# Performance work log

Measured on AMD Instinct MI355X. Metric: run time of the kernel, lower is better.

The kernel has to match this reference:

```python
import jax, jax.numpy as jnp
import numpy as np

V, D, H, DK, DV = 60000, 300, 15, 20, 20
B, NH, NC, L = 128, 50, 5, 30
HD = H * DV  # 300, equals d_model
A = 200      # additive attention hidden dim


def _encode(x, Wq, Wk, Wv, Wp, bp, qv):
    # NRMS news/user encoder: MHSA over positions + additive attention pooling.
    # x: [B, L, D] -> [B, HD]
    b, l, _ = x.shape
    q = (x @ Wq).reshape(b, l, H, DK)
    k = (x @ Wk).reshape(b, l, H, DK)
    v = (x @ Wv).reshape(b, l, H, DV)
    scores = jnp.einsum('blhk,bmhk->bhlm', q, k) / jnp.sqrt(jnp.asarray(DK, x.dtype))
    attn = jax.nn.softmax(scores, axis=-1)
    ctx = jnp.einsum('bhlm,bmhv->blhv', attn, v).reshape(b, l, HD)
    a = jax.nn.softmax(jnp.tanh(ctx @ Wp + bp) @ qv, axis=-1)  # [b, l]
    return jnp.einsum('bl,blc->bc', a, ctx)

# vectorize over the per-position encoder axis (replaces the Python loop +
# incremental torch.cat): inputs [B, P, L, D], weights have leading dim P.
_encode_pos = jax.vmap(_encode, in_axes=(1, 0, 0, 0, 0, 0, 0), out_axes=1)


def setup_inputs() -> dict:
    key = jax.random.key(0)
    ks = jax.random.split(key, 24)

    def mk(k, shape, s=0.02):
        return s * jax.random.normal(k, shape, jnp.float32)

    inp = {
        'news_input': jax.random.randint(ks[0], (B, NH, L), 0, V),
        'candidates': jax.random.randint(ks[1], (B, NC, L), 0, V),
        'emb': mk(ks[2], (V, D), 0.1),
    }
    for name, n, base in [('his', NH, 3), ('cand', NC, 10), ('usr', 0, 17)]:
        sh = (n,) if n else ()
        kk = jax.random.split(ks[base], 6)
        inp[name + '_Wq'] = mk(kk[0], sh + (D, H * DK))
        inp[name + '_Wk'] = mk(kk[1], sh + (D, H * DK))
        inp[name + '_Wv'] = mk(kk[2], sh + (D, H * DV))
        inp[name + '_Wp'] = mk(kk[3], sh + (HD, A))
        inp[name + '_bp'] = mk(kk[4], sh + (A,))
        inp[name + '_qv'] = mk(kk[5], sh + (A,))
    return inp


def reference(news_input, candidates, emb,
              his_Wq, his_Wk, his_Wv, his_Wp, his_bp, his_qv,
              cand_Wq, cand_Wk, cand_Wv, cand_Wp, cand_bp, cand_qv,
              usr_Wq, usr_Wk, usr_Wv, usr_Wp, usr_bp, usr_qv):
    news_emb = emb[news_input]   # [B, 50, L, D]
    cand_emb = emb[candidates]   # [B, 5, L, D]
    news_enc = _encode_pos(news_emb, his_Wq, his_Wk, his_Wv, his_Wp, his_bp, his_qv)    # [B, 50, 300]
    cand_enc = _encode_pos(cand_emb, cand_Wq, cand_Wk, cand_Wv, cand_Wp, cand_bp, cand_qv)  # [B, 5, 300]
    user_rep = _encode(news_enc, usr_Wq, usr_Wk, usr_Wv, usr_Wp, usr_bp, usr_qv)        # [B, 300]
    scores = jnp.einsum('bd,bcd->bc', user_rep, cand_enc)  # bmm of [B,1,300] x [B,300,5]
    return jax.nn.softmax(scores, axis=-1)
```

## Files before the change

kernel.cpp:

```cpp
#include <hip/hip_runtime.h>
#include <math.h>

typedef __attribute__((ext_vector_type(8))) short short8;
typedef __attribute__((ext_vector_type(4))) short short4v;
typedef __attribute__((ext_vector_type(4))) float f32x4;

union U32S8 { unsigned u[4]; short8 s8; ushort e[8]; short4v h[2]; };

#define BATCH 128
#define NHIS  50
#define NCAND 5
#define KP    320
#define NQKV  1024
#define NWP   208
#define NQK   640
#define CTS   320
#define VOCAB 60000
#define SCALE 0.22360679774997896f

__device__ __forceinline__ ushort f2bf(float f) {
    union { float f; unsigned u; } v; v.f = f;
    return (ushort)((v.u + 0x7fffu + ((v.u >> 16) & 1u)) >> 16);
}
__device__ __forceinline__ unsigned pack2bf(float lo, float hi) {
    return (unsigned)f2bf(lo) | ((unsigned)f2bf(hi) << 16);
}
__device__ __forceinline__ float bf2f(ushort u) {
    union { float f; unsigned u; } v; v.u = ((unsigned)u) << 16;
    return v.f;
}

__device__ __forceinline__ void gl_lds16(const ushort* gsrc, ushort* ldst) {
    __builtin_amdgcn_global_load_lds(
        (const __attribute__((address_space(1))) unsigned int*)gsrc,
        (__attribute__((address_space(3))) unsigned int*)ldst,
        16, 0, 0);
}

__global__ void prep_emb(const float* __restrict__ emb, ushort* __restrict__ dst) {
    size_t gid = (size_t)blockIdx.x * 256 + threadIdx.x;
    size_t total8 = (size_t)VOCAB * (KP / 8);
    if (gid >= total8) return;
    size_t e0 = gid * 8;
    int row = (int)(e0 / KP);
    int c   = (int)(e0 - (size_t)row * KP);
    unsigned w[4] = {0, 0, 0, 0};
    if (c + 8 <= 300) {
        const float4* s = (const float4*)(emb + (size_t)row * 300 + c);
        float4 v0 = s[0], v1 = s[1];
        w[0] = pack2bf(v0.x, v0.y); w[1] = pack2bf(v0.z, v0.w);
        w[2] = pack2bf(v1.x, v1.y); w[3] = pack2bf(v1.z, v1.w);
    } else if (c < 300) {
        const float* s = emb + (size_t)row * 300;
        ushort tmp[8];
        #pragma unroll
        for (int i = 0; i < 8; ++i) tmp[i] = (c + i < 300) ? f2bf(s[c + i]) : (ushort)0;
        w[0] = tmp[0] | ((unsigned)tmp[1] << 16);
        w[1] = tmp[2] | ((unsigned)tmp[3] << 16);
        w[2] = tmp[4] | ((unsigned)tmp[5] << 16);
        w[3] = tmp[6] | ((unsigned)tmp[7] << 16);
    }
    *(unsigned*)(dst + e0)     = w[0];
    *(unsigned*)(dst + e0 + 2) = w[1];
    *(unsigned*)(dst + e0 + 4) = w[2];
    *(unsigned*)(dst + e0 + 6) = w[3];
}

__global__ void prep_qkv(const float* __restrict__ Wq, const float* __restrict__ Wk,
                         const float* __restrict__ Wv, ushort* __restrict__ dst, int P) {
    size_t i = (size_t)blockIdx.x * 256 + threadIdx.x;
    size_t total = (size_t)P * NQKV * KP;
    if (i >= total) return;
    int k = (int)(i % KP);
    int n = (int)((i / KP) % NQKV);
    int p = (int)(i / ((size_t)KP * NQKV));
    float v = 0.f;
    if (k < 300 && n < 900) {
        const float* W = (n < 300) ? Wq : (n < 600 ? Wk : Wv);
        int nn = n % 300;
        v = W[((size_t)p * 300 + k) * 300 + nn];
    }
    dst[i] = f2bf(v);
}

__global__ void prep_wp(const float* __restrict__ Wp, ushort* __restrict__ dst, int P) {
    size_t i = (size_t)blockIdx.x * 256 + threadIdx.x;
    size_t total = (size_t)P * NWP * KP;
    if (i >= total) return;
    int k = (int)(i % KP);
    int a = (int)((i / KP) % NWP);
    int p = (int)(i / ((size_t)KP * NWP));
    float v = 0.f;
    if (k < 300 && a < 200) v = Wp[((size_t)p * 300 + k) * 200 + a];
    dst[i] = f2bf(v);
}

template<int LQ, bool GATHER>
__global__ __launch_bounds__(256, 4)
void qkv_gemm(const ushort* __restrict__ src_bf,
              const int* __restrict__ tokens,
              const ushort* __restrict__ wt,
              ushort* __restrict__ qk, ushort* __restrict__ vt,
              int p0, int P_all, int NPMT)
{
    constexpr int MT = (LQ == 30) ? 30 : 50;
    constexpr int VS = (LQ == 30) ? 32 : 64;
    constexpr int TS = 136;

    __shared__ __align__(16) char SM[34816];
    __shared__ int TOK[128];

    const int group = blockIdx.x >> 6;
    const int w64   = blockIdx.x & 63;
    const int mt_g  = group * 8 + (w64 & 7);
    const int ntile = w64 >> 3;
    if (mt_g >= NPMT) return;
    const int mtile = mt_g % MT;
    const int p_l   = mt_g / MT;
    const int p_g   = p0 + p_l;
    const int t     = threadIdx.x;
    const int wave  = t >> 6, lane = t & 63;
    const int r = lane & 15, g = lane >> 4;
    const int qm = wave >> 1, qn = wave & 1;

    if (GATHER && t < 128) {
        int row = mtile * 128 + t;
        int b = row / LQ, l = row - b * LQ;
        TOK[t] = tokens[((size_t)b * P_all + p_g) * LQ + l];
    }
    __syncthreads();

    const int kcs   = (lane & 3) ^ ((lane >> 2) & 3);
    const int rowA0 = wave * 16 + (lane >> 2);
    const int rowA1 = 64 + rowA0;
    const ushort* wtp = wt + (size_t)p_g * NQKV * KP;

    const ushort *pA0, *pA1;
    if (GATHER) {
        pA0 = src_bf + (size_t)TOK[rowA0] * KP + kcs * 8;
        pA1 = src_bf + (size_t)TOK[rowA1] * KP + kcs * 8;
    } else {
        pA0 = src_bf + (size_t)(mtile * 128 + rowA0) * KP + kcs * 8;
        pA1 = src_bf + (size_t)(mtile * 128 + rowA1) * KP + kcs * 8;
    }
    const ushort* pB0 = wtp + (size_t)(ntile * 128 + rowA0) * KP + kcs * 8;
    const ushort* pB1 = wtp + (size_t)(ntile * 128 + rowA1) * KP + kcs * 8;

    auto stage = [&](int ks, int bufb) {
        int ko = ks * 32;
        char* base = SM + bufb * 8192;
        gl_lds16(pA0 + ko, (ushort*)(base + wave * 1024));
        gl_lds16(pA1 + ko, (ushort*)(base + 4096 + wave * 1024));
        char* baseB = SM + 16384 + bufb * 8192;
        gl_lds16(pB0 + ko, (ushort*)(baseB + wave * 1024));
        gl_lds16(pB1 + ko, (ushort*)(baseB + 4096 + wave * 1024));
    };

    f32x4 acc[4][4];
    #pragma unroll
    for (int i = 0; i < 4; ++i)
        #pragma unroll
        for (int j = 0; j < 4; ++j)
            acc[i][j] = (f32x4){0.f, 0.f, 0.f, 0.f};

    stage(0, 0);
    __syncthreads();
    int buf = 0;
    const int kx = g ^ (r & 3);
    for (int ks = 0; ks < 10; ++ks) {
        if (ks < 9) stage(ks + 1, buf ^ 1);
        const ushort* Ab = (const ushort*)(SM + buf * 8192);
        const ushort* Bb = (const ushort*)(SM + 16384 + buf * 8192);
        short8 af[4], bfr[4];
        #pragma unroll
        for (int fi = 0; fi < 4; ++fi)
            af[fi] = *(const short8*)&Ab[(qm * 64 + fi * 16 + r) * 32 + kx * 8];
        #pragma unroll
        for (int fj = 0; fj < 4; ++fj)
            bfr[fj] = *(const short8*)&Bb[(qn * 64 + fj * 16 + r) * 32 + kx * 8];
        #pragma unroll
        for (int fi = 0; fi < 4; ++fi)
            #pragma unroll
            for (int fj = 0; fj < 4; ++fj)
                acc[fi][fj] = __builtin_amdgcn_mfma_f32_16x16x32_bf16(af[fi], bfr[fj], acc[fi][fj], 0, 0, 0);
        __syncthreads();
        buf ^= 1;
    }

    ushort* T = (ushort*)SM;
    #pragma unroll
    for (int fi = 0; fi < 4; ++fi) {
        #pragma unroll
        for (int fj = 0; fj < 4; ++fj) {
            int col  = qn * 64 + fj * 16 + r;
            int rowb = qm * 64 + fi * 16 + 4 * g;
            #pragma unroll
            for (int j = 0; j < 4; ++j)
                T[(rowb + j) * TS + col] = f2bf(acc[fi][fj][j]);
        }
    }
    __syncthreads();

    const int R0 = mtile * 128;
    const int N0 = ntile * 128;
    ushort* qkp = qk + (size_t)p_l * (128 * MT) * NQK;
    ushort* vtp = vt + (size_t)p_l * BATCH * 15 * 20 * VS;

    {
        int nqk = 600 - N0;
        if (nqk > 128) nqk = 128;
        if (nqk > 0) {
            int nch = nqk >> 3;
            for (int t2 = t; t2 < 128 * nch; t2 += 256) {
                int row = t2 / nch, cc = t2 - row * nch;
                short8 v = *(const short8*)&T[row * TS + cc * 8];
                *(short8*)&qkp[(size_t)(R0 + row) * NQK + N0 + cc * 8] = v;
            }
        }
    }
    {
        int c0 = 600 - N0; if (c0 < 0) c0 = 0;
        int c1 = 900 - N0; if (c1 > 128) c1 = 128;
        if (c1 > c0) {
            int nvt = c1 - c0;
            int b0 = R0 / LQ, b1 = (R0 + 127) / LQ;
            int nb = b1 - b0 + 1;
            for (int t2 = t; t2 < nvt * nb; t2 += 256) {
                int ci = t2 % nvt, bi = t2 / nvt;
                int c = c0 + ci;
                int vj = N0 + c - 600;
                int h = vj / 20, jj = vj - h * 20;
                int b = b0 + bi;
                int gr0 = b * LQ;      if (gr0 < R0) gr0 = R0;
                int gr1 = b * LQ + LQ; if (gr1 > R0 + 128) gr1 = R0 + 128;
                if (gr1 <= gr0) continue;
                int l0 = gr0 - b * LQ, l1 = gr1 - b * LQ;
                ushort* dst = vtp + (((size_t)b * 15 + h) * 20 + jj) * VS;
                int l = l0;
                while (l < l1) {
                    if ((l & 7) == 0 && l + 8 <= l1) {
                        U32S8 v;
                        #pragma unroll
                        for (int i = 0; i < 8; ++i)
                            v.e[i] = T[(b * LQ + l + i - R0) * TS + c];
                        *(short8*)&dst[l] = v.s8;
                        l += 8;
                    } else if ((l & 1) == 0 && l + 2 <= l1) {
                        unsigned v = (unsigned)T[(b * LQ + l - R0) * TS + c] |
                                     ((unsigned)T[(b * LQ + l + 1 - R0) * TS + c] << 16);
                        *(unsigned*)&dst[l] = v;
                        l += 2;
                    } else {
                        dst[l] = T[(b * LQ + l - R0) * TS + c];
                        l += 1;
                    }
                }
            }
        }
    }
}

__device__ __forceinline__ short8 load_qk_frag(const ushort* rowptr, int colbase, int g, bool rowvalid) {
    U32S8 v;
    v.s8 = (short8){0,0,0,0,0,0,0,0};
    if (rowvalid && g < 3) {
        const ushort* src = rowptr + colbase;
        if (g < 2) {
            v.h[0] = *(const short4v*)src;
            v.h[1] = *(const short4v*)(src + 4);
        } else {
            v.h[0] = *(const short4v*)src;
        }
    }
    return v.s8;
}

template<bool BF16OUT>
__global__ __launch_bounds__(256, 4)
void attn_pool30(const ushort* __restrict__ qk,
                 const ushort* __restrict__ vt,
                 const ushort* __restrict__ wt_wp,
                 const float* __restrict__ bp, const float* __restrict__ qv,
                 float* __restrict__ outf, ushort* __restrict__ outbf,
                 int p0, int P_all)
{
    constexpr int CS = 328;
    __shared__ ushort C[32 * CS];
    __shared__ float  SL[32];
    __shared__ float  AW[32];

    const int tid  = threadIdx.x;
    const int wave = tid >> 6;
    const int lane = tid & 63;
    const int r = lane & 15, g = lane >> 4;
    const int p_l = blockIdx.x / BATCH;
    const int b   = blockIdx.x % BATCH;
    const int p_g = p0 + p_l;

    const ushort* qb  = qk + ((size_t)p_l * BATCH + b) * 30 * NQK;
    const ushort* vb  = vt + ((size_t)p_l * BATCH + b) * 15 * 640;
    const ushort* wpp = wt_wp + (size_t)p_g * NWP * KP;

    for (int i = tid; i < 32 * CS / 8; i += 256) {
        short8 z = (short8){0,0,0,0,0,0,0,0};
        *(short8*)&C[i * 8] = z;
    }
    if (tid < 32) SL[tid] = 0.f;
    __syncthreads();

    for (int hp = 0; hp < 4; ++hp) {
        int head = wave + 4 * hp;
        if (head < 15) {
            short8 q0 = load_qk_frag(qb + (size_t)(r) * NQK,      head * 20 + 8 * g, g, r < 30);
            short8 q1 = load_qk_frag(qb + (size_t)(16 + r) * NQK, head * 20 + 8 * g, g, 16 + r < 30);
            short8 k0 = load_qk_frag(qb + (size_t)(r) * NQK,      300 + head * 20 + 8 * g, g, r < 30);
            short8 k1 = load_qk_frag(qb + (size_t)(16 + r) * NQK, 300 + head * 20 + 8 * g, g, 16 + r < 30);
            short8 vf0 = *(const short8*)&vb[head * 640 + r * 32 + 8 * g];
            short8 vf1 = (16 + r < 20) ? *(const short8*)&vb[head * 640 + (16 + r) * 32 + 8 * g]
                                       : (short8){0,0,0,0,0,0,0,0};

            f32x4 s0m0 = {0,0,0,0}, s0m1 = {0,0,0,0}, s1m0 = {0,0,0,0}, s1m1 = {0,0,0,0};
            s0m0 = __builtin_amdgcn_mfma_f32_16x16x32_bf16(k0, q0, s0m0, 0, 0, 0);
            s0m1 = __builtin_amdgcn_mfma_f32_16x16x32_bf16(k1, q0, s0m1, 0, 0, 0);
            s1m0 = __builtin_amdgcn_mfma_f32_16x16x32_bf16(k0, q1, s1m0, 0, 0, 0);
            s1m1 = __builtin_amdgcn_mfma_f32_16x16x32_bf16(k1, q1, s1m1, 0, 0, 0);

            float mx0 = -1e30f, mx1 = -1e30f;
            #pragma unroll
            for (int j = 0; j < 4; ++j) {
                s0m0[j] *= SCALE; s1m0[j] *= SCALE;
                float v01 = (16 + 4 * g + j < 30) ? s0m1[j] * SCALE : -1e30f;
                float v11 = (16 + 4 * g + j < 30) ? s1m1[j] * SCALE : -1e30f;
                s0m1[j] = v01; s1m1[j] = v11;
                mx0 = fmaxf(mx0, fmaxf(s0m0[j], v01));
                mx1 = fmaxf(mx1, fmaxf(s1m0[j], v11));
            }
            mx0 = fmaxf(mx0, __shfl_xor(mx0, 16, 64));
            mx0 = fmaxf(mx0, __shfl_xor(mx0, 32, 64));
            mx1 = fmaxf(mx1, __shfl_xor(mx1, 16, 64));
            mx1 = fmaxf(mx1, __shfl_xor(mx1, 32, 64));
            float sm0 = 0.f, sm1 = 0.f;
            #pragma unroll
            for (int j = 0; j < 4; ++j) {
                s0m0[j] = __expf(s0m0[j] - mx0); s0m1[j] = __expf(s0m1[j] - mx0);
                s1m0[j] = __expf(s1m0[j] - mx1); s1m1[j] = __expf(s1m1[j] - mx1);
                sm0 += s0m0[j] + s0m1[j];
                sm1 += s1m0[j] + s1m1[j];
            }
            sm0 += __shfl_xor(sm0, 16, 64); sm0 += __shfl_xor(sm0, 32, 64);
            sm1 += __shfl_xor(sm1, 16, 64); sm1 += __shfl_xor(sm1, 32, 64);
            float inv0 = 1.0f / sm0, inv1 = 1.0f / sm1;

            unsigned pk000 = pack2bf(s0m0[0] * inv0, s0m0[1] * inv0);
            unsigned pk001 = pack2bf(s0m0[2] * inv0, s0m0[3] * inv0);
            unsigned pk010 = pack2bf(s0m1[0] * inv0, s0m1[1] * inv0);
            unsigned pk011 = pack2bf(s0m1[2] * inv0, s0m1[3] * inv0);
            unsigned pk100 = pack2bf(s1m0[0] * inv1, s1m0[1] * inv1);
            unsigned pk101 = pack2bf(s1m0[2] * inv1, s1m0[3] * inv1);
            unsigned pk110 = pack2bf(s1m1[0] * inv1, s1m1[1] * inv1);
            unsigned pk111 = pack2bf(s1m1[2] * inv1, s1m1[3] * inv1);

            const int sA = r + 16 * (2 * (g & 1));
            const int sB = sA + 16;
            const bool hi = (g >> 1) != 0;
            #pragma unroll
            for (int lt = 0; lt < 2; ++lt) {
                unsigned q00 = lt ? pk100 : pk000, q01 = lt ? pk101 : pk001;
                unsigned q10 = lt ? pk110 : pk010, q11 = lt ? pk111 : pk011;
                unsigned a0 = __shfl((int)q00, sA, 64), a1 = __shfl((int)q01, sA, 64);
                unsigned a2 = __shfl((int)q10, sA, 64), a3 = __shfl((int)q11, sA, 64);
                unsigned b0 = __shfl((int)q00, sB, 64), b1 = __shfl((int)q01, sB, 64);
                unsigned b2 = __shfl((int)q10, sB, 64), b3 = __shfl((int)q11, sB, 64);
                U32S8 pf;
                pf.u[0] = hi ? a2 : a0;
                pf.u[1] = hi ? a3 : a1;
                pf.u[2] = hi ? b2 : b0;
                pf.u[3] = hi ? b3 : b1;
                int lrow = lt * 16 + r;
                #pragma unroll
                for (int nt = 0; nt < 2; ++nt) {
                    short8 vf = nt ? vf1 : vf0;
                    f32x4 c = {0.f, 0.f, 0.f, 0.f};
                    c = __builtin_amdgcn_mfma_f32_16x16x32_bf16(vf, pf.s8, c, 0, 0, 0);
                    if (lrow < 30) {
                        #pragma unroll
                        for (int j = 0; j < 4; ++j) {
                            int vj = nt * 16 + 4 * g + j;
                            if (vj < 20)
                                C[lrow * CS + head * 20 + vj] = f2bf(c[j]);
                        }
                    }
                }
            }
        }
    }
    __syncthreads();

    for (int nt = wave; nt < 13; nt += 4) {
        int col = nt * 16 + r;
        const ushort* wrow = wpp + (size_t)col * KP + 8 * g;
        short8 breg[10];
        #pragma unroll
        for (int ks = 0; ks < 10; ++ks) breg[ks] = *(const short8*)(wrow + 32 * ks);
        float bpv = (col < 200) ? bp[p_g * 200 + col] : 0.f;
        float qvv = (col < 200) ? qv[p_g * 200 + col] : 0.f;

        f32x4 acc0 = {0.f, 0.f, 0.f, 0.f}, acc1 = {0.f, 0.f, 0.f, 0.f};
        #pragma unroll
        for (int ks = 0; ks < 10; ++ks) {
            short8 a0 = *(const short8*)&C[(r) * CS + ks * 32 + 8 * g];
            short8 a1 = *(const short8*)&C[(16 + r) * CS + ks * 32 + 8 * g];
            acc0 = __builtin_amdgcn_mfma_f32_16x16x32_bf16(a0, breg[ks], acc0, 0, 0, 0);
            acc1 = __builtin_amdgcn_mfma_f32_16x16x32_bf16(a1, breg[ks], acc1, 0, 0, 0);
        }
        #pragma unroll
        for (int j = 0; j < 4; ++j) {
            float s0 = tanhf(acc0[j] + bpv) * qvv;
            float s1 = tanhf(acc1[j] + bpv) * qvv;
            s0 += __shfl_xor(s0, 1, 64); s1 += __shfl_xor(s1, 1, 64);
            s0 += __shfl_xor(s0, 2, 64); s1 += __shfl_xor(s1, 2, 64);
            s0 += __shfl_xor(s0, 4, 64); s1 += __shfl_xor(s1, 4, 64);
            s0 += __shfl_xor(s0, 8, 64); s1 += __shfl_xor(s1, 8, 64);
            if (r == 0) {
                atomicAdd(&SL[4 * g + j], s0);
                atomicAdd(&SL[16 + 4 * g + j], s1);
            }
        }
    }
    __syncthreads();

    if (wave == 0) {
        float x = (lane < 30) ? SL[lane] : -1e30f;
        float mx = x;
        #pragma unroll
        for (int off = 1; off < 64; off <<= 1) mx = fmaxf(mx, __shfl_xor(mx, off, 64));
        float e = (lane < 30) ? __expf(x - mx) : 0.f;
        float sm = e;
        #pragma unroll
        for (int off = 1; off < 64; off <<= 1) sm += __shfl_xor(sm, off, 64);
        if (lane < 32) AW[lane] = e / sm;
    }
    __syncthreads();

    for (int c = tid; c < 300; c += 256) {
        float o = 0.f;
        #pragma unroll
        for (int l = 0; l < 30; ++l)
            o = fmaf(AW[l], bf2f(C[l * CS + c]), o);
        if (BF16OUT) outbf[((size_t)b * P_all + p_g) * KP + c] = f2bf(o);
        else         outf[((size_t)b * P_all + p_g) * 300 + c] = o;
    }
}

__global__ __launch_bounds__(512, 1)
void attn50(const ushort* __restrict__ qk,
            const ushort* __restrict__ vt,
            ushort* __restrict__ ctx)
{
    __shared__ ushort P_l[8][64 * 68];

    const int tid  = threadIdx.x;
    const int wave = tid >> 6;
    const int lane = tid & 63;
    const int r = lane & 15, g = lane >> 4;
    const int b = blockIdx.x;

    const ushort* qb = qk + (size_t)b * 50 * NQK;
    ushort* pw = &P_l[wave][0];

    for (int hh = wave; hh < 15; hh += 8) {
        short8 qf[4], kf[4];
        #pragma unroll
        for (int t4 = 0; t4 < 4; ++t4) {
            qf[t4] = load_qk_frag(qb + (size_t)(t4 * 16 + r) * NQK, hh * 20 + 8 * g, g, true);
            kf[t4] = load_qk_frag(qb + (size_t)(t4 * 16 + r) * NQK, 300 + hh * 20 + 8 * g, g, true);
        }
        short8 vf[2][2];
        #pragma unroll
        for (int nt = 0; nt < 2; ++nt) {
            int vj = nt * 16 + r;
            #pragma unroll
            for (int ks = 0; ks < 2; ++ks) {
                if (vj < 20)
                    vf[nt][ks] = *(const short8*)&vt[(((size_t)b * 15 + hh) * 20 + vj) * 64 + ks * 32 + 8 * g];
                else
                    vf[nt][ks] = (short8){0,0,0,0,0,0,0,0};
            }
        }

        f32x4 s[4][4];
        #pragma unroll
        for (int qt = 0; qt < 4; ++qt)
            #pragma unroll
            for (int kt = 0; kt < 4; ++kt) {
                f32x4 z = {0.f, 0.f, 0.f, 0.f};
                s[qt][kt] = __builtin_amdgcn_mfma_f32_16x16x32_bf16(kf[kt], qf[qt], z, 0, 0, 0);
            }

        float mx[4], sm[4];
        #pragma unroll
        for (int qt = 0; qt < 4; ++qt) {
            float m = -1e30f;
            #pragma unroll
            for (int kt = 0; kt < 4; ++kt)
                #pragma unroll
                for (int j = 0; j < 4; ++j) {
                    int col = kt * 16 + 4 * g + j;
                    float v = (col < 50) ? s[qt][kt][j] * SCALE : -1e30f;
                    s[qt][kt][j] = v;
                    m = fmaxf(m, v);
                }
            m = fmaxf(m, __shfl_xor(m, 16, 64));
            m = fmaxf(m, __shfl_xor(m, 32, 64));
            mx[qt] = m;
            float sum = 0.f;
            #pragma unroll
            for (int kt = 0; kt < 4; ++kt)
                #pragma unroll
                for (int j = 0; j < 4; ++j) {
                    float e = __expf(s[qt][kt][j] - m);
                    s[qt][kt][j] = e;
                    sum += e;
                }
            sum += __shfl_xor(sum, 16, 64);
            sum += __shfl_xor(sum, 32, 64);
            sm[qt] = 1.0f / sum;
        }

        #pragma unroll
        for (int qt = 0; qt < 4; ++qt) {
            float inv = sm[qt];
            #pragma unroll
            for (int kt = 0; kt < 4; ++kt) {
                unsigned w0 = pack2bf(s[qt][kt][0] * inv, s[qt][kt][1] * inv);
                unsigned w1 = pack2bf(s[qt][kt][2] * inv, s[qt][kt][3] * inv);
                ushort* dst = pw + (qt * 16 + r) * 68 + kt * 16 + 4 * g;
                *(unsigned*)dst = w0;
                *(unsigned*)(dst + 2) = w1;
            }
        }
        asm volatile("s_waitcnt lgkmcnt(0)");
        __builtin_amdgcn_sched_barrier(0);

        #pragma unroll
        for (int lt = 0; lt < 4; ++lt) {
            short8 pf0 = *(const short8*)(pw + (lt * 16 + r) * 68 + 8 * g);
            short8 pf1 = *(const short8*)(pw + (lt * 16 + r) * 68 + 32 + 8 * g);
            int l = lt * 16 + r;
            #pragma unroll
            for (int nt = 0; nt < 2; ++nt) {
                f32x4 c = {0.f, 0.f, 0.f, 0.f};
                c = __builtin_amdgcn_mfma_f32_16x16x32_bf16(vf[nt][0], pf0, c, 0, 0, 0);
                c = __builtin_amdgcn_mfma_f32_16x16x32_bf16(vf[nt][1], pf1, c, 0, 0, 0);
                int vjb = nt * 16 + 4 * g;
                if (l < 50 && vjb < 17) {
                    unsigned w0 = pack2bf(c[0], c[1]);
                    unsigned w1 = pack2bf(c[2], c[3]);
                    ushort* d = ctx + ((size_t)b * 64 + l) * CTS + hh * 20 + vjb;
                    *(unsigned*)d = w0;
                    *(unsigned*)(d + 2) = w1;
                }
            }
        }
    }
}

__global__ __launch_bounds__(256, 2)
void pool50(const ushort* __restrict__ ctx,
            const ushort* __restrict__ wt_wp,
            const float* __restrict__ bp, const float* __restrict__ qv,
            float* __restrict__ user_rep)
{
    __shared__ ushort Bt[2][208 * 40];
    __shared__ float  logit[128];
    __shared__ float  aw[128];

    const int tid  = threadIdx.x;
    const int wave = tid >> 6;
    const int lane = tid & 63;
    const int r = lane & 15, g = lane >> 4;

    const ushort* cbase = ctx + (size_t)blockIdx.x * 2 * 64 * CTS;

    auto stageB = [&](int ks, int buf) {
        for (int i = tid; i < 832; i += 256) {
            int n = i >> 2, kk = (i & 3) * 8;
            *(short8*)&Bt[buf][n * 40 + kk] = *(const short8*)&wt_wp[(size_t)n * KP + ks * 32 + kk];
        }
    };

    float bpr[13], qvr[13];
    #pragma unroll
    for (int nf = 0; nf < 13; ++nf) {
        int col = nf * 16 + r;
        bpr[nf] = (col < 200) ? bp[col] : 0.f;
        qvr[nf] = (col < 200) ? qv[col] : 0.f;
    }

    f32x4 acc[2][13];
    #pragma unroll
    for (int mf = 0; mf < 2; ++mf)
        #pragma unroll
        for (int nf = 0; nf < 13; ++nf)
            acc[mf][nf] = (f32x4){0.f, 0.f, 0.f, 0.f};

    stageB(0, 0);
    __syncthreads();
    int buf = 0;
    for (int ks = 0; ks < 10; ++ks) {
        if (ks < 9) stageB(ks + 1, buf ^ 1);
        short8 af[2];
        #pragma unroll
        for (int mf = 0; mf < 2; ++mf)
            af[mf] = *(const short8*)&cbase[(size_t)(wave * 32 + mf * 16 + r) * CTS + ks * 32 + 8 * g];
        #pragma unroll
        for (int mf = 0; mf < 2; ++mf)
            #pragma unroll
            for (int nf = 0; nf < 13; ++nf) {
                short8 bf = *(const short8*)&Bt[buf][(nf * 16 + r) * 40 + 8 * g];
                acc[mf][nf] = __builtin_amdgcn_mfma_f32_16x16x32_bf16(af[mf], bf, acc[mf][nf], 0, 0, 0);
            }
        __syncthreads();
        buf ^= 1;
    }

    #pragma unroll
    for (int mf = 0; mf < 2; ++mf) {
        #pragma unroll
        for (int j = 0; j < 4; ++j) {
            float s = 0.f;
            #pragma unroll
            for (int nf = 0; nf < 13; ++nf)
                s += tanhf(acc[mf][nf][j] + bpr[nf]) * qvr[nf];
            s += __shfl_xor(s, 1, 64);
            s += __shfl_xor(s, 2, 64);
            s += __shfl_xor(s, 4, 64);
            s += __shfl_xor(s, 8, 64);
            if (r == 0) logit[wave * 32 + mf * 16 + 4 * g + j] = s;
        }
    }
    __syncthreads();

    if (wave < 2) {
        float x = (lane < 50) ? logit[wave * 64 + lane] : -1e30f;
        float mx = x;
        #pragma unroll
        for (int off = 1; off < 64; off <<= 1) mx = fmaxf(mx, __shfl_xor(mx, off, 64));
        float e = (lane < 50) ? __expf(x - mx) : 0.f;
        float sm = e;
        #pragma unroll
        for (int off = 1; off < 64; off <<= 1) sm += __shfl_xor(sm, off, 64);
        aw[wave * 64 + lane] = e / sm;
    }
    __syncthreads();

    for (int idx = tid; idx < 2 * 300; idx += 256) {
        int inst = idx / 300, c = idx - inst * 300;
        const ushort* crow = cbase + (size_t)inst * 64 * CTS + c;
        float o = 0.f;
        #pragma unroll
        for (int l = 0; l < 50; ++l)
            o = fmaf(aw[inst * 64 + l], bf2f(crow[(size_t)l * CTS]), o);
        int b = blockIdx.x * 2 + inst;
        user_rep[(size_t)b * 300 + c] = o;
    }
}

__global__ __launch_bounds__(320)
void score_kernel(const float* __restrict__ user_rep, const float* __restrict__ cand_enc,
                  float* __restrict__ out)
{
    __shared__ float sc[NCAND];
    int b = blockIdx.x;
    int w = threadIdx.x >> 6;
    int lane = threadIdx.x & 63;
    float partial = 0.f;
    for (int d = lane; d < 300; d += 64)
        partial = fmaf(user_rep[b * 300 + d], cand_enc[((size_t)b * NCAND + w) * 300 + d], partial);
    for (int off = 32; off > 0; off >>= 1)
        partial += __shfl_down(partial, off, 64);
    if (lane == 0) sc[w] = partial;
    __syncthreads();
    if (threadIdx.x == 0) {
        float mx = -1e30f;
        for (int c = 0; c < NCAND; ++c) mx = fmaxf(mx, sc[c]);
        float s = 0.f; float e[NCAND];
        for (int c = 0; c < NCAND; ++c) { e[c] = __expf(sc[c] - mx); s += e[c]; }
        float inv = 1.0f / s;
        for (int c = 0; c < NCAND; ++c) out[b * NCAND + c] = e[c] * inv;
    }
}

extern "C" void kernel_launch(void* const* d_in, const int* in_sizes, int n_in,
                              void* d_out, int out_size, void* d_ws, size_t ws_size,
                              hipStream_t stream) {
    const int*   news_input = (const int*)d_in[0];
    const int*   candidates = (const int*)d_in[1];
    const float* emb        = (const float*)d_in[2];
    const float* his_Wq  = (const float*)d_in[3];
    const float* his_Wk  = (const float*)d_in[4];
    const float* his_Wv  = (const float*)d_in[5];
    const float* his_Wp  = (const float*)d_in[6];
    const float* his_bp  = (const float*)d_in[7];
    const float* his_qv  = (const float*)d_in[8];
    const float* cand_Wq = (const float*)d_in[9];
    const float* cand_Wk = (const float*)d_in[10];
    const float* cand_Wv = (const float*)d_in[11];
    const float* cand_Wp = (const float*)d_in[12];
    const float* cand_bp = (const float*)d_in[13];
    const float* cand_qv = (const float*)d_in[14];
    const float* usr_Wq  = (const float*)d_in[15];
    const float* usr_Wk  = (const float*)d_in[16];
    const float* usr_Wv  = (const float*)d_in[17];
    const float* usr_Wp  = (const float*)d_in[18];
    const float* usr_bp  = (const float*)d_in[19];
    const float* usr_qv  = (const float*)d_in[20];
    float* out = (float*)d_out;

    char* ws = (char*)d_ws;
    ushort* emb_bf      = (ushort*)ws;            ws += (size_t)VOCAB * KP * 2;
    ushort* news_enc_bf = (ushort*)ws;            ws += (size_t)BATCH * NHIS * KP * 2;
    float* cand_enc = (float*)ws;                 ws += (size_t)BATCH * NCAND * 300 * 4;
    float* user_rep = (float*)ws;                 ws += (size_t)BATCH * 300 * 4;
    ushort* his_qkvT  = (ushort*)ws;              ws += (size_t)NHIS * NQKV * KP * 2;
    ushort* his_wpT   = (ushort*)ws;              ws += (size_t)NHIS * NWP  * KP * 2;
    ushort* cand_qkvT = (ushort*)ws;              ws += (size_t)NCAND * NQKV * KP * 2;
    ushort* cand_wpT  = (ushort*)ws;              ws += (size_t)NCAND * NWP  * KP * 2;
    ushort* usr_qkvT  = (ushort*)ws;              ws += (size_t)NQKV * KP * 2;
    ushort* usr_wpT   = (ushort*)ws;              ws += (size_t)NWP  * KP * 2;

    size_t used = (size_t)(ws - (char*)d_ws);
    size_t avail = (ws_size > used) ? (ws_size - used) : 0;
    size_t qk_pp  = (size_t)3840 * NQK * 2;
    size_t vt_pp  = (size_t)BATCH * 15 * 640 * 2;
    size_t per_p  = qk_pp + vt_pp;
    int CP = (int)(avail / per_p);
    if (CP > 50) CP = 50;
    if (CP < 3) CP = 3;

    ushort* qk_ws  = (ushort*)ws;
    ushort* vt_ws  = qk_ws + (size_t)CP * 3840 * NQK;

    ushort* qk_u  = qk_ws;
    ushort* vt_u  = qk_u + (size_t)6400 * NQK;
    ushort* ctx_u = vt_u + (size_t)BATCH * 15 * 20 * 64;

    auto blocks = [](size_t total) { return (int)((total + 255) / 256); };
    auto qkv_grid = [](int npmt) { return ((npmt + 7) / 8) * 64; };

    hipMemsetAsync(news_enc_bf, 0, (size_t)BATCH * NHIS * KP * 2, stream);
    prep_emb<<<blocks((size_t)VOCAB * (KP / 8)), 256, 0, stream>>>(emb, emb_bf);
    prep_qkv<<<blocks((size_t)NHIS  * NQKV * KP), 256, 0, stream>>>(his_Wq,  his_Wk,  his_Wv,  his_qkvT,  NHIS);
    prep_qkv<<<blocks((size_t)NCAND * NQKV * KP), 256, 0, stream>>>(cand_Wq, cand_Wk, cand_Wv, cand_qkvT, NCAND);
    prep_qkv<<<blocks((size_t)1     * NQKV * KP), 256, 0, stream>>>(usr_Wq,  usr_Wk,  usr_Wv,  usr_qkvT,  1);
    prep_wp <<<blocks((size_t)NHIS  * NWP  * KP), 256, 0, stream>>>(his_Wp,  his_wpT,  NHIS);
    prep_wp <<<blocks((size_t)NCAND * NWP  * KP), 256, 0, stream>>>(cand_Wp, cand_wpT, NCAND);
    prep_wp <<<blocks((size_t)1     * NWP  * KP), 256, 0, stream>>>(usr_Wp,  usr_wpT,  1);

    for (int p0 = 0; p0 < NHIS; p0 += CP) {
        int cp = (NHIS - p0 < CP) ? (NHIS - p0) : CP;
        int npmt = cp * 30;
        qkv_gemm<30, true><<<qkv_grid(npmt), 256, 0, stream>>>(emb_bf, news_input, his_qkvT,
                                                               qk_ws, vt_ws, p0, NHIS, npmt);
        attn_pool30<true><<<cp * BATCH, 256, 0, stream>>>(qk_ws, vt_ws, his_wpT, his_bp, his_qv,
                                                          nullptr, news_enc_bf, p0, NHIS);
    }
    {
        int npmt = NCAND * 30;
        qkv_gemm<30, true><<<qkv_grid(npmt), 256, 0, stream>>>(emb_bf, candidates, cand_qkvT,
                                                               qk_ws, vt_ws, 0, NCAND, npmt);
        attn_pool30<false><<<NCAND * BATCH, 256, 0, stream>>>(qk_ws, vt_ws, cand_wpT, cand_bp, cand_qv,
                                                              cand_enc, nullptr, 0, NCAND);
    }

    hipMemsetAsync(vt_u, 0, (size_t)BATCH * 15 * 20 * 64 * 2, stream);
    qkv_gemm<50, false><<<qkv_grid(50), 256, 0, stream>>>(news_enc_bf, nullptr, usr_qkvT,
                                                          qk_u, vt_u, 0, 1, 50);
    attn50<<<BATCH, 512, 0, stream>>>(qk_u, vt_u, ctx_u);
    pool50<<<64, 256, 0, stream>>>(ctx_u, usr_wpT, usr_bp, usr_qv, user_rep);

    score_kernel<<<BATCH, 320, 0, stream>>>(user_rep, cand_enc, out);
}
```

Before: 804.8 us.

## Store Q and K in head-major contiguous layout for attention kernels

The QKV GEMM epilogue now writes Q and K into separate per-(batch, head) tiles of [L,20] bf16 instead of row-major [rows,640] with Q and K interleaved by column. The attention kernels (attn_pool30, attn50) read each head's Q/K fragments from contiguous 20-element rows, which should improve the locality of global loads. The intermediate footprint shrinks from 640 to 600 columns per row. In exchange, the epilogue scatter is more complex, with per-head vector-width branching and smaller stores.

```diff
diff --git a/kernel.cpp b/kernel.cpp
--- a/kernel.cpp
+++ b/kernel.cpp
@@ -13,7 +13,6 @@
 #define KP    320
 #define NQKV  1024
 #define NWP   208
-#define NQK   640
 #define CTS   320
 #define VOCAB 60000
 #define SCALE 0.22360679774997896f
@@ -35,6 +34,21 @@
         (const __attribute__((address_space(1))) unsigned int*)gsrc,
         (__attribute__((address_space(3))) unsigned int*)ldst,
         16, 0, 0);
+}
+
+__device__ __forceinline__ short8 load_h20(const ushort* tile20, int row, int g, bool rowvalid) {
+    U32S8 v;
+    v.s8 = (short8){0,0,0,0,0,0,0,0};
+    if (rowvalid && g < 3) {
+        const ushort* src = tile20 + row * 20 + 8 * g;
+        if (g < 2) {
+            v.h[0] = *(const short4v*)src;
+            v.h[1] = *(const short4v*)(src + 4);
+        } else {
+            v.h[0] = *(const short4v*)src;
+        }
+    }
+    return v.s8;
 }
 
 __global__ void prep_emb(const float* __restrict__ emb, ushort* __restrict__ dst) {
@@ -100,7 +114,7 @@
 void qkv_gemm(const ushort* __restrict__ src_bf,
               const int* __restrict__ tokens,
               const ushort* __restrict__ wt,
-              ushort* __restrict__ qk, ushort* __restrict__ vt,
+              ushort* __restrict__ qh, ushort* __restrict__ kh, ushort* __restrict__ vt,
               int p0, int P_all, int NPMT)
 {
     constexpr int MT = (LQ == 30) ? 30 : 50;
@@ -203,18 +217,52 @@
 
     const int R0 = mtile * 128;
     const int N0 = ntile * 128;
-    ushort* qkp = qk + (size_t)p_l * (128 * MT) * NQK;
+    ushort* qhp = qh + (size_t)p_l * BATCH * 15 * LQ * 20;
+    ushort* khp = kh + (size_t)p_l * BATCH * 15 * LQ * 20;
     ushort* vtp = vt + (size_t)p_l * BATCH * 15 * 20 * VS;
 
-    {
-        int nqk = 600 - N0;
-        if (nqk > 128) nqk = 128;
-        if (nqk > 0) {
-            int nch = nqk >> 3;
-            for (int t2 = t; t2 < 128 * nch; t2 += 256) {
-                int row = t2 / nch, cc = t2 - row * nch;
-                short8 v = *(const short8*)&T[row * TS + cc * 8];
-                *(short8*)&qkp[(size_t)(R0 + row) * NQK + N0 + cc * 8] = v;
+    #pragma unroll
+    for (int seg = 0; seg < 2; ++seg) {
+        int nlo = seg * 300;
+        int lo = (N0 > nlo) ? N0 : nlo;
+        int hi = ((N0 + 128) < (nlo + 300)) ? (N0 + 128) : (nlo + 300);
+        if (hi <= lo) continue;
+        int h0 = (lo - nlo) / 20;
+        int h1 = (hi - 1 - nlo) / 20;
+        int nh = h1 - h0 + 1;
+        ushort* dstb = seg ? khp : qhp;
+        for (int t2 = t; t2 < 128 * nh; t2 += 256) {
+            int hh = t2 % nh, row = t2 / nh;
+            int h = h0 + hh;
+            int nA = nlo + 20 * h;
+            int j0 = (lo > nA) ? (lo - nA) : 0;
+            int j1 = ((nA + 20) < hi ? (nA + 20) : hi) - nA;
+            int grow = R0 + row;
+            int b = grow / LQ, l = grow - b * LQ;
+            ushort* dst = dstb + (((size_t)b * 15 + h) * LQ + l) * 20;
+            const ushort* srcT = &T[row * TS + (nA + j0 - N0)];
+            int j = j0;
+            while (j < j1) {
+                if ((j & 7) == 0 && j + 8 <= j1) {
+                    U32S8 v;
+                    #pragma unroll
+                    for (int i = 0; i < 8; ++i) v.e[i] = srcT[j - j0 + i];
+                    *(short8*)&dst[j] = v.s8;
+                    j += 8;
+                } else if ((j & 3) == 0 && j + 4 <= j1) {
+                    U32S8 v;
+                    #pragma unroll
+                    for (int i = 0; i < 4; ++i) v.e[i] = srcT[j - j0 + i];
+                    *(short4v*)&dst[j] = v.h[0];
+                    j += 4;
+                } else if ((j & 1) == 0 && j + 2 <= j1) {
+                    unsigned v = (unsigned)srcT[j - j0] | ((unsigned)srcT[j - j0 + 1] << 16);
+                    *(unsigned*)&dst[j] = v;
+                    j += 2;
+                } else {
+                    dst[j] = srcT[j - j0];
+                    j += 1;
+                }
             }
         }
     }
@@ -260,24 +308,10 @@
     }
 }
 
-__device__ __forceinline__ short8 load_qk_frag(const ushort* rowptr, int colbase, int g, bool rowvalid) {
-    U32S8 v;
-    v.s8 = (short8){0,0,0,0,0,0,0,0};
-    if (rowvalid && g < 3) {
-        const ushort* src = rowptr + colbase;
-        if (g < 2) {
-            v.h[0] = *(const short4v*)src;
-            v.h[1] = *(const short4v*)(src + 4);
-        } else {
-            v.h[0] = *(const short4v*)src;
-        }
-    }
-    return v.s8;
-}
-
 template<bool BF16OUT>
 __global__ __launch_bounds__(256, 4)
-void attn_pool30(const ushort* __restrict__ qk,
+void attn_pool30(const ushort* __restrict__ qh,
+                 const ushort* __restrict__ kh,
                  const ushort* __restrict__ vt,
                  const ushort* __restrict__ wt_wp,
                  const float* __restrict__ bp, const float* __restrict__ qv,
@@ -297,7 +331,8 @@
     const int b   = blockIdx.x % BATCH;
     const int p_g = p0 + p_l;
 
-    const ushort* qb  = qk + ((size_t)p_l * BATCH + b) * 30 * NQK;
+    const ushort* qb  = qh + (((size_t)p_l * BATCH + b) * 15) * 600;
+    const ushort* kb  = kh + (((size_t)p_l * BATCH + b) * 15) * 600;
     const ushort* vb  = vt + ((size_t)p_l * BATCH + b) * 15 * 640;
     const ushort* wpp = wt_wp + (size_t)p_g * NWP * KP;
 
@@ -311,10 +346,12 @@
     for (int hp = 0; hp < 4; ++hp) {
         int head = wave + 4 * hp;
         if (head < 15) {
-            short8 q0 = load_qk_frag(qb + (size_t)(r) * NQK,      head * 20 + 8 * g, g, r < 30);
-            short8 q1 = load_qk_frag(qb + (size_t)(16 + r) * NQK, head * 20 + 8 * g, g, 16 + r < 30);
-            short8 k0 = load_qk_frag(qb + (size_t)(r) * NQK,      300 + head * 20 + 8 * g, g, r < 30);
-            short8 k1 = load_qk_frag(qb + (size_t)(16 + r) * NQK, 300 + head * 20 + 8 * g, g, 16 + r < 30);
+            const ushort* qt = qb + head * 600;
+            const ushort* kt = kb + head * 600;
+            short8 q0 = load_h20(qt, r, g, true);
+            short8 q1 = load_h20(qt, 16 + r, g, 16 + r < 30);
+            short8 k0 = load_h20(kt, r, g, true);
+            short8 k1 = load_h20(kt, 16 + r, g, 16 + r < 30);
             short8 vf0 = *(const short8*)&vb[head * 640 + r * 32 + 8 * g];
             short8 vf1 = (16 + r < 20) ? *(const short8*)&vb[head * 640 + (16 + r) * 32 + 8 * g]
                                        : (short8){0,0,0,0,0,0,0,0};
@@ -453,7 +490,8 @@
 }
 
 __global__ __launch_bounds__(512, 1)
-void attn50(const ushort* __restrict__ qk,
+void attn50(const ushort* __restrict__ qh,
+            const ushort* __restrict__ kh,
             const ushort* __restrict__ vt,
             ushort* __restrict__ ctx)
 {
@@ -465,15 +503,16 @@
     const int r = lane & 15, g = lane >> 4;
     const int b = blockIdx.x;
 
-    const ushort* qb = qk + (size_t)b * 50 * NQK;
     ushort* pw = &P_l[wave][0];
 
     for (int hh = wave; hh < 15; hh += 8) {
+        const ushort* qt = qh + (((size_t)b * 15 + hh) * 50) * 20;
+        const ushort* kt = kh + (((size_t)b * 15 + hh) * 50) * 20;
         short8 qf[4], kf[4];
         #pragma unroll
         for (int t4 = 0; t4 < 4; ++t4) {
-            qf[t4] = load_qk_frag(qb + (size_t)(t4 * 16 + r) * NQK, hh * 20 + 8 * g, g, true);
-            kf[t4] = load_qk_frag(qb + (size_t)(t4 * 16 + r) * NQK, 300 + hh * 20 + 8 * g, g, true);
+            qf[t4] = load_h20(qt, t4 * 16 + r, g, true);
+            kf[t4] = load_h20(kt, t4 * 16 + r, g, true);
         }
         short8 vf[2][2];
         #pragma unroll
@@ -490,51 +529,51 @@
 
         f32x4 s[4][4];
         #pragma unroll
-        for (int qt = 0; qt < 4; ++qt)
-            #pragma unroll
-            for (int kt = 0; kt < 4; ++kt) {
+        for (int qt2 = 0; qt2 < 4; ++qt2)
+            #pragma unroll
+            for (int kt2 = 0; kt2 < 4; ++kt2) {
                 f32x4 z = {0.f, 0.f, 0.f, 0.f};
-                s[qt][kt] = __builtin_amdgcn_mfma_f32_16x16x32_bf16(kf[kt], qf[qt], z, 0, 0, 0);
+                s[qt2][kt2] = __builtin_amdgcn_mfma_f32_16x16x32_bf16(kf[kt2], qf[qt2], z, 0, 0, 0);
             }
 
         float mx[4], sm[4];
         #pragma unroll
-        for (int qt = 0; qt < 4; ++qt) {
+        for (int qt2 = 0; qt2 < 4; ++qt2) {
             float m = -1e30f;
             #pragma unroll
-            for (int kt = 0; kt < 4; ++kt)
+            for (int kt2 = 0; kt2 < 4; ++kt2)
                 #pragma unroll
                 for (int j = 0; j < 4; ++j) {
-                    int col = kt * 16 + 4 * g + j;
-                    float v = (col < 50) ? s[qt][kt][j] * SCALE : -1e30f;
-                    s[qt][kt][j] = v;
+                    int col = kt2 * 16 + 4 * g + j;
+                    float v = (col < 50) ? s[qt2][kt2][j] * SCALE : -1e30f;
+                    s[qt2][kt2][j] = v;
                     m = fmaxf(m, v);
                 }
             m = fmaxf(m, __shfl_xor(m, 16, 64));
             m = fmaxf(m, __shfl_xor(m, 32, 64));
-            mx[qt] = m;
+            mx[qt2] = m;
             float sum = 0.f;
             #pragma unroll
-            for (int kt = 0; kt < 4; ++kt)
+            for (int kt2 = 0; kt2 < 4; ++kt2)
                 #pragma unroll
                 for (int j = 0; j < 4; ++j) {
-                    float e = __expf(s[qt][kt][j] - m);
-                    s[qt][kt][j] = e;
+                    float e = __expf(s[qt2][kt2][j] - m);
+                    s[qt2][kt2][j] = e;
                     sum += e;
                 }
             sum += __shfl_xor(sum, 16, 64);
             sum += __shfl_xor(sum, 32, 64);
-            sm[qt] = 1.0f / sum;
-        }
-
-        #pragma unroll
-        for (int qt = 0; qt < 4; ++qt) {
-            float inv = sm[qt];
-            #pragma unroll
-            for (int kt = 0; kt < 4; ++kt) {
-                unsigned w0 = pack2bf(s[qt][kt][0] * inv, s[qt][kt][1] * inv);
-                unsigned w1 = pack2bf(s[qt][kt][2] * inv, s[qt][kt][3] * inv);
-                ushort* dst = pw + (qt * 16 + r) * 68 + kt * 16 + 4 * g;
+            sm[qt2] = 1.0f / sum;
+        }
+
+        #pragma unroll
+        for (int qt2 = 0; qt2 < 4; ++qt2) {
+            float inv = sm[qt2];
+            #pragma unroll
+            for (int kt2 = 0; kt2 < 4; ++kt2) {
+                unsigned w0 = pack2bf(s[qt2][kt2][0] * inv, s[qt2][kt2][1] * inv);
+                unsigned w1 = pack2bf(s[qt2][kt2][2] * inv, s[qt2][kt2][3] * inv);
+                ushort* dst = pw + (qt2 * 16 + r) * 68 + kt2 * 16 + 4 * g;
                 *(unsigned*)dst = w0;
                 *(unsigned*)(dst + 2) = w1;
             }
@@ -731,18 +770,20 @@
 
     size_t used = (size_t)(ws - (char*)d_ws);
     size_t avail = (ws_size > used) ? (ws_size - used) : 0;
-    size_t qk_pp  = (size_t)3840 * NQK * 2;
-    size_t vt_pp  = (size_t)BATCH * 15 * 640 * 2;
-    size_t per_p  = qk_pp + vt_pp;
+    size_t qh_pp = (size_t)BATCH * 15 * 30 * 20 * 2;
+    size_t vt_pp = (size_t)BATCH * 15 * 640 * 2;
+    size_t per_p = 2 * qh_pp + vt_pp;
     int CP = (int)(avail / per_p);
     if (CP > 50) CP = 50;
-    if (CP < 3) CP = 3;
-
-    ushort* qk_ws  = (ushort*)ws;
-    ushort* vt_ws  = qk_ws + (size_t)CP * 3840 * NQK;
-
-    ushort* qk_u  = qk_ws;
-    ushort* vt_u  = qk_u + (size_t)6400 * NQK;
+    if (CP < 4) CP = 4;
+
+    ushort* qh_ws = (ushort*)ws;
+    ushort* kh_ws = qh_ws + (size_t)CP * BATCH * 15 * 30 * 20;
+    ushort* vt_ws = kh_ws + (size_t)CP * BATCH * 15 * 30 * 20;
+
+    ushort* qh_u  = qh_ws;
+    ushort* kh_u  = qh_u + (size_t)BATCH * 15 * 50 * 20 + 2048;
+    ushort* vt_u  = kh_u + (size_t)BATCH * 15 * 50 * 20 + 2048;
     ushort* ctx_u = vt_u + (size_t)BATCH * 15 * 20 * 64;
 
     auto blocks = [](size_t total) { return (int)((total + 255) / 256); };
@@ -761,22 +802,22 @@
         int cp = (NHIS - p0 < CP) ? (NHIS - p0) : CP;
         int npmt = cp * 30;
         qkv_gemm<30, true><<<qkv_grid(npmt), 256, 0, stream>>>(emb_bf, news_input, his_qkvT,
-                                                               qk_ws, vt_ws, p0, NHIS, npmt);
-        attn_pool30<true><<<cp * BATCH, 256, 0, stream>>>(qk_ws, vt_ws, his_wpT, his_bp, his_qv,
+                                                               qh_ws, kh_ws, vt_ws, p0, NHIS, npmt);
+        attn_pool30<true><<<cp * BATCH, 256, 0, stream>>>(qh_ws, kh_ws, vt_ws, his_wpT, his_bp, his_qv,
                                                           nullptr, news_enc_bf, p0, NHIS);
     }
     {
         int npmt = NCAND * 30;
         qkv_gemm<30, true><<<qkv_grid(npmt), 256, 0, stream>>>(emb_bf, candidates, cand_qkvT,
-                                                               qk_ws, vt_ws, 0, NCAND, npmt);
-        attn_pool30<false><<<NCAND * BATCH, 256, 0, stream>>>(qk_ws, vt_ws, cand_wpT, cand_bp, cand_qv,
+                                                               qh_ws, kh_ws, vt_ws, 0, NCAND, npmt);
+        attn_pool30<false><<<NCAND * BATCH, 256, 0, stream>>>(qh_ws, kh_ws, vt_ws, cand_wpT, cand_bp, cand_qv,
                                                               cand_enc, nullptr, 0, NCAND);
     }
 
     hipMemsetAsync(vt_u, 0, (size_t)BATCH * 15 * 20 * 64 * 2, stream);
     qkv_gemm<50, false><<<qkv_grid(50), 256, 0, stream>>>(news_enc_bf, nullptr, usr_qkvT,
-                                                          qk_u, vt_u, 0, 1, 50);
-    attn50<<<BATCH, 512, 0, stream>>>(qk_u, vt_u, ctx_u);
+                                                          qh_u, kh_u, vt_u, 0, 1, 50);
+    attn50<<<BATCH, 512, 0, stream>>>(qh_u, kh_u, vt_u, ctx_u);
     pool50<<<64, 256, 0, stream>>>(ctx_u, usr_wpT, usr_bp, usr_qv, user_rep);
 
     score_kernel<<<BATCH, 320, 0, stream>>>(user_rep, cand_enc, out);
```

Measured after the change: 824.9 us. +2.5%, slower.
